# Kernel optimization log

Hardware: AMD Instinct MI355X
Metric: run time of the kernel (lower is better)

Reference implementation:

```python
import jax, jax.numpy as jnp
import numpy as np
import math

B, T, D, H, E, K = 2, 2048, 1024, 16, 8, 2
F = 4 * D
HD = D // H
EPS = 1e-5


def layer_norm(x, w):
    mu = jnp.mean(x, axis=-1, keepdims=True)
    var = jnp.mean(jnp.square(x - mu), axis=-1, keepdims=True)
    return (x - mu) / jnp.sqrt(var + EPS) * w


def setup_inputs() -> dict:
    key = jax.random.key(0)
    ks = jax.random.split(key, 8)
    s = 0.02
    return {
        "x": jax.random.normal(ks[0], (B, T, D), dtype=jnp.float32),
        "ln1_w": jnp.ones((D,), dtype=jnp.float32),
        "wqkv": jax.random.normal(ks[1], (D, 3 * D), dtype=jnp.float32) * s,
        "wproj": jax.random.normal(ks[2], (D, D), dtype=jnp.float32) * s,
        "ln2_w": jnp.ones((D,), dtype=jnp.float32),
        "router_w": jax.random.normal(ks[3], (D, E), dtype=jnp.float32) * s,
        "w1": jax.random.normal(ks[4], (E, D, F), dtype=jnp.float32) * s,
        "w2": jax.random.normal(ks[5], (E, F, D), dtype=jnp.float32) * s,
    }


def reference(x, ln1_w, wqkv, wproj, ln2_w, router_w, w1, w2):
    # --- self-attention (causal, no bias, dropout=0, eval mode) ---
    h = layer_norm(x, ln1_w)
    qkv = h @ wqkv  # [B,T,3D]
    q, k, v = jnp.split(qkv, 3, axis=-1)
    q = q.reshape(B, T, H, HD).transpose(0, 2, 1, 3)  # [B,H,T,HD]
    k = k.reshape(B, T, H, HD).transpose(0, 2, 1, 3)
    v = v.reshape(B, T, H, HD).transpose(0, 2, 1, 3)
    scores = jnp.einsum("bhqd,bhkd->bhqk", q, k) / math.sqrt(HD)
    causal = jnp.tril(jnp.ones((T, T), dtype=bool))
    scores = jnp.where(causal, scores, jnp.float32(-1e9))
    attn = jax.nn.softmax(scores, axis=-1)
    o = jnp.einsum("bhqk,bhkd->bhqd", attn, v)
    o = o.transpose(0, 2, 1, 3).reshape(B, T, D) @ wproj
    x = x + o

    # --- pre-MoE norm (note: residual for MoE uses ln2 output, per source) ---
    x = layer_norm(x, ln2_w)

    # --- router (eval mode: top-k of softmax probs) ---
    logits = x @ router_w  # [B,T,E]
    probs = jax.nn.softmax(logits, axis=-1)
    _, topi = jax.lax.top_k(probs, K)  # [B,T,K]
    mask = jax.nn.one_hot(topi, E, dtype=probs.dtype).sum(axis=-2)  # [B,T,E]
    rp = probs * mask
    rp = rp / jnp.sum(rp, axis=-1, keepdims=True)  # normalize=True, top_k>1

    # --- experts: dense-equivalent of gather/MLP/scatter (zero-prob tokens contribute 0) ---
    hh = jax.nn.gelu(jnp.einsum("btd,edf->ebtf", x, w1), approximate=False)
    eo = jnp.einsum("ebtf,efd->ebtd", hh, w2)
    next_states = jnp.einsum("bte,ebtd->btd", rp, eo)
    return x + next_states
```

## Files before the change

kernel.cpp:

```cpp
#include <hip/hip_runtime.h>
#include <hip/hip_bf16.h>
#include <math.h>

#define Bv 2
#define Tv 2048
#define Dv 1024
#define Hv 16
#define Ev 8
#define Kv 2
#define Fv 4096
#define HDv 64
#define NT 4096
#define MAXTILES 72

typedef __attribute__((ext_vector_type(8))) short short8;
typedef __attribute__((ext_vector_type(4))) float f32x4;

__device__ __forceinline__ short f2bf(float f) {
  unsigned u = __builtin_bit_cast(unsigned, f);
  u += 0x7fffu + ((u >> 16) & 1u);
  return (short)(u >> 16);
}
__device__ __forceinline__ float bf2f(short s) {
  unsigned u = ((unsigned)(unsigned short)s) << 16;
  return __builtin_bit_cast(float, u);
}
__device__ __forceinline__ float wredsum(float s) {
  #pragma unroll
  for (int off = 32; off; off >>= 1) s += __shfl_down(s, off, 64);
  return s;
}
__device__ __forceinline__ void gl_lds16(const short* g, short* l) {
  __builtin_amdgcn_global_load_lds(
      (const __attribute__((address_space(1))) unsigned int*)g,
      (__attribute__((address_space(3))) unsigned int*)l, 16, 0, 0);
}

__global__ __launch_bounds__(256) void transpose_cvt(const float* __restrict__ in,
                                                     short* __restrict__ out,
                                                     int Kd, int Nd) {
  __shared__ float tile[64][65];
  const float* inb = in + (size_t)blockIdx.z * Kd * Nd;
  short* outb = out + (size_t)blockIdx.z * Kd * Nd;
  const int k0 = blockIdx.x * 64, n0 = blockIdx.y * 64;
  const int rr = threadIdx.x >> 4, cc = (threadIdx.x & 15) * 4;
  #pragma unroll
  for (int i = 0; i < 4; i++) {
    int r = rr + i * 16;
    f32x4 v = *(const f32x4*)(inb + (size_t)(k0 + r) * Nd + n0 + cc);
    tile[r][cc] = v[0]; tile[r][cc + 1] = v[1];
    tile[r][cc + 2] = v[2]; tile[r][cc + 3] = v[3];
  }
  __syncthreads();
  #pragma unroll
  for (int i = 0; i < 2; i++) {
    int e = threadIdx.x + i * 256;
    int n = e >> 3, c = (e & 7) * 8;
    short8 v;
    #pragma unroll
    for (int j = 0; j < 8; j++) v[j] = f2bf(tile[c + j][n]);
    *(short8*)(outb + (size_t)(n0 + n) * Kd + k0 + c) = v;
  }
}

__global__ __launch_bounds__(256) void vtrans_kernel(const short* __restrict__ qkv,
                                                     short* __restrict__ vT) {
  __shared__ short tile[64][72];
  const int t0 = blockIdx.x * 64;
  const int bh = blockIdx.y;
  const int b = bh >> 4, h = bh & 15;
  #pragma unroll
  for (int i = 0; i < 2; i++) {
    int e = threadIdx.x + i * 256;
    int r = e >> 3, c = (e & 7) * 8;
    short8 v = *(const short8*)(qkv + (size_t)(b * Tv + t0 + r) * 3072 + 2048 + h * 64 + c);
    *(short8*)(&tile[r][c]) = v;
  }
  __syncthreads();
  #pragma unroll
  for (int i = 0; i < 2; i++) {
    int e = threadIdx.x + i * 256;
    int d = e >> 3, c = (e & 7) * 8;
    short8 v;
    #pragma unroll
    for (int j = 0; j < 8; j++) v[j] = tile[c + j][d];
    *(short8*)(vT + ((size_t)bh * 64 + d) * Tv + t0 + c) = v;
  }
}

__global__ __launch_bounds__(256) void ln_kernel(const float* __restrict__ in,
                                                 const float* __restrict__ w,
                                                 float* __restrict__ outf,
                                                 short* __restrict__ outb) {
  int t = blockIdx.x;
  int tid = threadIdx.x;
  const float* row = in + (size_t)t * Dv;
  float v[4]; float s = 0.f;
  #pragma unroll
  for (int i = 0; i < 4; i++) { v[i] = row[tid + i * 256]; s += v[i]; }
  s = wredsum(s);
  __shared__ float red[4], red2[4];
  int wv = tid >> 6, ln = tid & 63;
  if (ln == 0) red[wv] = s;
  __syncthreads();
  float mu = (red[0] + red[1] + red[2] + red[3]) * (1.f / Dv);
  float vs = 0.f;
  #pragma unroll
  for (int i = 0; i < 4; i++) { float d = v[i] - mu; vs += d * d; }
  vs = wredsum(vs);
  if (ln == 0) red2[wv] = vs;
  __syncthreads();
  float var = (red2[0] + red2[1] + red2[2] + red2[3]) * (1.f / Dv);
  float inv = rsqrtf(var + 1e-5f);
  #pragma unroll
  for (int i = 0; i < 4; i++) {
    int d = tid + i * 256;
    float o = (v[i] - mu) * inv * w[d];
    if (outf) outf[(size_t)t * Dv + d] = o;
    if (outb) outb[(size_t)t * Dv + d] = f2bf(o);
  }
}

enum { EPI_BF16 = 0, EPI_RESID = 1, EPI_GELU = 2, EPI_F32 = 3 };

template<int EPI, bool MOE, bool INDIRECT>
__global__ __launch_bounds__(256) void gemm_lds(
    const short* __restrict__ A, const short* __restrict__ Bt,
    short* __restrict__ Cb, float* __restrict__ Cf,
    const float* __restrict__ resid,
    const int* __restrict__ perm, const int* __restrict__ tiles,
    int M, int N, int K) {
  __shared__ short As[128][32];
  __shared__ short Bs[128][32];
  const int nwg = gridDim.x * gridDim.y;
  const int orig = blockIdx.y * gridDim.x + blockIdx.x;
  const int cpx = nwg >> 3;
  const int wgid = (orig & 7) * cpx + (orig >> 3);
  const int mt = wgid % gridDim.x;
  const int npan = wgid / gridDim.x;

  int row0, row_end;
  const short* Bp = Bt;
  if (MOE) {
    int ntile = tiles[0];
    if (mt >= ntile) return;
    int e   = tiles[1 + mt * 3];
    row0    = tiles[2 + mt * 3];
    row_end = tiles[3 + mt * 3];
    Bp = Bt + (size_t)e * K * N;
  } else {
    row0 = mt * 128; row_end = M;
  }
  const int nbase = npan * 128;
  const int tid = threadIdx.x;
  const int lane = tid & 63;
  const int w = tid >> 6;
  const int wm = (w >> 1) * 64, wn = (w & 1) * 64;
  const int lr = lane & 15, lk = (lane >> 4) * 8;

  const int lrow = lane >> 2, lcol = (lane & 3) * 8;
  const short* asrc[2]; short* adst[2];
  const short* bsrc[2]; short* bdst[2];
  #pragma unroll
  for (int i = 0; i < 2; i++) {
    int grow = row0 + w * 16 + i * 64 + lrow;
    if (MOE) grow = min(grow, row_end - 1);
    int arow = INDIRECT ? perm[grow] : grow;
    asrc[i] = A + (size_t)arow * K + lcol;
    adst[i] = &As[w * 16 + i * 64][0];
    bsrc[i] = Bp + (size_t)(nbase + w * 16 + i * 64 + lrow) * K + lcol;
    bdst[i] = &Bs[w * 16 + i * 64][0];
  }

  f32x4 acc[4][4];
  #pragma unroll
  for (int m = 0; m < 4; m++)
    #pragma unroll
    for (int n = 0; n < 4; n++) acc[m][n] = (f32x4)0.0f;

  for (int k0 = 0; k0 < K; k0 += 32) {
    #pragma unroll
    for (int i = 0; i < 2; i++) {
      gl_lds16(asrc[i] + k0, adst[i]);
      gl_lds16(bsrc[i] + k0, bdst[i]);
    }
    __syncthreads();
    short8 af[4], bfr[4];
    #pragma unroll
    for (int m = 0; m < 4; m++) af[m] = *(const short8*)(&As[wm + m * 16 + lr][lk]);
    #pragma unroll
    for (int n = 0; n < 4; n++) bfr[n] = *(const short8*)(&Bs[wn + n * 16 + lr][lk]);
    #pragma unroll
    for (int m = 0; m < 4; m++)
      #pragma unroll
      for (int n = 0; n < 4; n++)
        acc[m][n] = __builtin_amdgcn_mfma_f32_16x16x32_bf16(af[m], bfr[n], acc[m][n], 0, 0, 0);
    __syncthreads();
  }
  #pragma unroll
  for (int m = 0; m < 4; m++) {
    #pragma unroll
    for (int n = 0; n < 4; n++) {
      #pragma unroll
      for (int r = 0; r < 4; r++) {
        int row = row0 + wm + m * 16 + (lane >> 4) * 4 + r;
        if (MOE && row >= row_end) continue;
        int col = nbase + wn + n * 16 + lr;
        float v = acc[m][n][r];
        size_t idx = (size_t)row * N + col;
        if (EPI == EPI_BF16) {
          Cb[idx] = f2bf(v);
        } else if (EPI == EPI_RESID) {
          Cf[idx] = v + resid[idx];
        } else if (EPI == EPI_GELU) {
          float g = 0.5f * v * (1.0f + erff(v * 0.70710678118f));
          Cb[idx] = f2bf(g);
        } else {
          Cf[idx] = v;
        }
      }
    }
  }
}

#define SCL2E 0.18033688011112042f

__global__ __launch_bounds__(256) void attn_kernel(const short* __restrict__ qkv,
                                                   const short* __restrict__ vT,
                                                   short* __restrict__ o) {
  const int qbase = ((int)gridDim.x - 1 - (int)blockIdx.x) * 64;
  const int bh = blockIdx.y;
  const int b = bh >> 4, h = bh & 15;
  const int w = threadIdx.x >> 6, lane = threadIdx.x & 63;
  const int lr = lane & 15, lkg = lane >> 4, lk = lkg * 8;
  const size_t rs = 3 * Dv;

  __shared__ short Ks[64][72];
  __shared__ short Vs[64][72];
  __shared__ short Ps[4][16][72];

  short8 qf[2];
  {
    size_t qrow = (size_t)(b * Tv + qbase + w * 16 + lr) * rs + h * 64;
    qf[0] = *(const short8*)(qkv + qrow + lk);
    qf[1] = *(const short8*)(qkv + qrow + 32 + lk);
  }
  f32x4 oacc[4];
  #pragma unroll
  for (int n = 0; n < 4; n++) oacc[n] = (f32x4)0.0f;
  float mrow[4] = {-INFINITY, -INFINITY, -INFINITY, -INFINITY};
  float lrow4[4] = {0.f, 0.f, 0.f, 0.f};

  const short* kbase = qkv + (size_t)b * Tv * rs + Dv + h * 64;
  const short* vbase = vT + (size_t)bh * 64 * Tv;

  for (int kv0 = 0; kv0 < qbase + 64; kv0 += 64) {
    #pragma unroll
    for (int i = 0; i < 2; i++) {
      int e = threadIdx.x + i * 256;
      int r = e >> 3, c = (e & 7) * 8;
      short8 kval = *(const short8*)(kbase + (size_t)(kv0 + r) * rs + c);
      *(short8*)(&Ks[r][c]) = kval;
      short8 vval = *(const short8*)(vbase + (size_t)r * Tv + kv0 + c);
      *(short8*)(&Vs[r][c]) = vval;
    }
    __syncthreads();
    f32x4 s[4];
    #pragma unroll
    for (int n = 0; n < 4; n++) {
      s[n] = (f32x4)0.0f;
      short8 kf0 = *(const short8*)(&Ks[n * 16 + lr][lk]);
      short8 kf1 = *(const short8*)(&Ks[n * 16 + lr][32 + lk]);
      s[n] = __builtin_amdgcn_mfma_f32_16x16x32_bf16(qf[0], kf0, s[n], 0, 0, 0);
      s[n] = __builtin_amdgcn_mfma_f32_16x16x32_bf16(qf[1], kf1, s[n], 0, 0, 0);
    }
    if (kv0 < qbase) {
      #pragma unroll
      for (int n = 0; n < 4; n++)
        #pragma unroll
        for (int r = 0; r < 4; r++) s[n][r] *= SCL2E;
    } else {
      #pragma unroll
      for (int n = 0; n < 4; n++)
        #pragma unroll
        for (int r = 0; r < 4; r++) {
          int tq = qbase + w * 16 + lkg * 4 + r;
          int tk = kv0 + n * 16 + lr;
          s[n][r] = (tk > tq) ? -1e30f : s[n][r] * SCL2E;
        }
    }
    float scr[4];
    #pragma unroll
    for (int r = 0; r < 4; r++) {
      float m = fmaxf(fmaxf(s[0][r], s[1][r]), fmaxf(s[2][r], s[3][r]));
      #pragma unroll
      for (int off = 8; off; off >>= 1) m = fmaxf(m, __shfl_xor(m, off, 64));
      float mnew = fmaxf(mrow[r], m);
      float sc = exp2f(mrow[r] - mnew);
      float rsum = 0.f;
      #pragma unroll
      for (int n = 0; n < 4; n++) { float p = exp2f(s[n][r] - mnew); s[n][r] = p; rsum += p; }
      #pragma unroll
      for (int off = 8; off; off >>= 1) rsum += __shfl_xor(rsum, off, 64);
      lrow4[r] = lrow4[r] * sc + rsum;
      mrow[r] = mnew;
      scr[r] = sc;
    }
    #pragma unroll
    for (int n = 0; n < 4; n++)
      #pragma unroll
      for (int r = 0; r < 4; r++) Ps[w][lkg * 4 + r][n * 16 + lr] = f2bf(s[n][r]);
    #pragma unroll
    for (int n = 0; n < 4; n++)
      #pragma unroll
      for (int r = 0; r < 4; r++) oacc[n][r] *= scr[r];
    __syncthreads();
    #pragma unroll
    for (int n2 = 0; n2 < 4; n2++) {
      short8 pf0 = *(const short8*)(&Ps[w][lr][lk]);
      short8 pf1 = *(const short8*)(&Ps[w][lr][32 + lk]);
      short8 vf0 = *(const short8*)(&Vs[n2 * 16 + lr][lk]);
      short8 vf1 = *(const short8*)(&Vs[n2 * 16 + lr][32 + lk]);
      oacc[n2] = __builtin_amdgcn_mfma_f32_16x16x32_bf16(pf0, vf0, oacc[n2], 0, 0, 0);
      oacc[n2] = __builtin_amdgcn_mfma_f32_16x16x32_bf16(pf1, vf1, oacc[n2], 0, 0, 0);
    }
    __syncthreads();
  }
  float rinv[4];
  #pragma unroll
  for (int r = 0; r < 4; r++) rinv[r] = 1.0f / lrow4[r];
  #pragma unroll
  for (int n2 = 0; n2 < 4; n2++)
    #pragma unroll
    for (int r = 0; r < 4; r++) {
      int tq = qbase + w * 16 + lkg * 4 + r;
      float v = oacc[n2][r] * rinv[r];
      o[(size_t)(b * Tv + tq) * Dv + h * 64 + n2 * 16 + lr] = f2bf(v);
    }
}

__global__ __launch_bounds__(256) void router_kernel(const float* __restrict__ x2f,
                                                     const float* __restrict__ rw,
                                                     int* __restrict__ topi,
                                                     float* __restrict__ topp) {
  int w = threadIdx.x >> 6, lane = threadIdx.x & 63;
  int t = blockIdx.x * 4 + w;
  const float* row = x2f + (size_t)t * Dv;
  float acc[8];
  #pragma unroll
  for (int e = 0; e < 8; e++) acc[e] = 0.f;
  for (int i = 0; i < 16; i++) {
    int d = lane + i * 64;
    float xv = row[d];
    const float* rwp = rw + (size_t)d * 8;
    #pragma unroll
    for (int e = 0; e < 8; e++) acc[e] += xv * rwp[e];
  }
  #pragma unroll
  for (int e = 0; e < 8; e++) acc[e] = wredsum(acc[e]);
  if (lane == 0) {
    float mx = acc[0];
    #pragma unroll
    for (int e = 1; e < 8; e++) mx = fmaxf(mx, acc[e]);
    float p[8]; float se = 0.f;
    #pragma unroll
    for (int e = 0; e < 8; e++) { p[e] = expf(acc[e] - mx); se += p[e]; }
    #pragma unroll
    for (int e = 0; e < 8; e++) p[e] /= se;
    int i1 = 0; float p1 = p[0];
    #pragma unroll
    for (int e = 1; e < 8; e++) if (p[e] > p1) { p1 = p[e]; i1 = e; }
    float pm = p[i1]; p[i1] = -1.f;
    int i2 = 0; float p2 = p[0];
    #pragma unroll
    for (int e = 1; e < 8; e++) if (p[e] > p2) { p2 = p[e]; i2 = e; }
    float sum = pm + p2;
    topi[t * 2] = i1; topi[t * 2 + 1] = i2;
    topp[t * 2] = pm / sum; topp[t * 2 + 1] = p2 / sum;
  }
}

__global__ void bucket_count(const int* __restrict__ topi, int* __restrict__ offsets,
                             int* __restrict__ cursor) {
  __shared__ int cnt[8];
  if (threadIdx.x < 8) { cnt[threadIdx.x] = 0; cursor[threadIdx.x] = 0; }
  __syncthreads();
  for (int i = threadIdx.x; i < NT * 2; i += 256) atomicAdd(&cnt[topi[i]], 1);
  __syncthreads();
  if (threadIdx.x == 0) {
    int s = 0;
    for (int e = 0; e < 8; e++) { offsets[e] = s; s += cnt[e]; }
    offsets[8] = s;
  }
}
__global__ void bucket_scatter(const int* __restrict__ topi, const int* __restrict__ offsets,
                               int* __restrict__ cursor, int* __restrict__ perm,
                               int* __restrict__ row_of) {
  int i = blockIdx.x * 256 + threadIdx.x;
  if (i >= NT * 2) return;
  int e = topi[i];
  int slot = atomicAdd(&cursor[e], 1);
  int r = offsets[e] + slot;
  perm[r] = i >> 1;
  row_of[i] = r;
}
__global__ void tile_build(const int* __restrict__ offsets, int* __restrict__ tiles) {
  if (threadIdx.x == 0 && blockIdx.x == 0) {
    int nt = 0;
    for (int e = 0; e < 8; e++) {
      int r0 = offsets[e], r1 = offsets[e + 1];
      for (int m = r0; m < r1; m += 128) {
        tiles[1 + nt * 3] = e; tiles[2 + nt * 3] = m; tiles[3 + nt * 3] = r1; nt++;
      }
    }
    tiles[0] = nt;
  }
}

__global__ __launch_bounds__(256) void final_kernel(float* __restrict__ out,
                                                    const short* __restrict__ eout,
                                                    const int* __restrict__ row_of,
                                                    const float* __restrict__ topp) {
  int t = blockIdx.x; int tid = threadIdx.x;
  int r0 = row_of[t * 2], r1 = row_of[t * 2 + 1];
  float p0 = topp[t * 2], p1 = topp[t * 2 + 1];
  #pragma unroll
  for (int i = 0; i < 4; i++) {
    int d = tid + i * 256;
    out[(size_t)t * Dv + d] += p0 * bf2f(eout[(size_t)r0 * Dv + d])
                             + p1 * bf2f(eout[(size_t)r1 * Dv + d]);
  }
}

extern "C" void kernel_launch(void* const* d_in, const int* in_sizes, int n_in,
                              void* d_out, int out_size, void* d_ws, size_t ws_size,
                              hipStream_t stream) {
  const float* x        = (const float*)d_in[0];
  const float* ln1_w    = (const float*)d_in[1];
  const float* wqkv     = (const float*)d_in[2];
  const float* wproj    = (const float*)d_in[3];
  const float* ln2_w    = (const float*)d_in[4];
  const float* router_w = (const float*)d_in[5];
  const float* w1       = (const float*)d_in[6];
  const float* w2       = (const float*)d_in[7];
  float* out = (float*)d_out;
  char* ws = (char*)d_ws;

  size_t off = 0;
  short* wqkvT  = (short*)(ws + off); off += (size_t)3 * Dv * Dv * 2;
  short* wprojT = (short*)(ws + off); off += (size_t)Dv * Dv * 2;
  short* w1T    = (short*)(ws + off); off += (size_t)Ev * Dv * Fv * 2;
  short* w2T    = (short*)(ws + off); off += (size_t)Ev * Fv * Dv * 2;
  char* reg1 = ws + off; off += (size_t)NT * Dv * 2;
  short* hln1 = (short*)reg1;
  short* ob   = (short*)reg1;
  short* x2b  = (short*)reg1;
  char* reg2 = ws + off; off += (size_t)NT * 3 * Dv * 2;
  short* qkvb = (short*)reg2;
  float* xres = (float*)reg2;
  char* reg3 = ws + off; off += (size_t)NT * 2 * Fv * 2;
  short* vT = (short*)reg3;
  short* Hb = (short*)reg3;
  short* eout = (short*)(ws + off); off += (size_t)NT * 2 * Dv * 2;
  int*   topi = (int*)(ws + off);   off += NT * 2 * 4;
  float* topp = (float*)(ws + off); off += NT * 2 * 4;
  int*   offs = (int*)(ws + off);   off += 64;
  int*   cur  = (int*)(ws + off);   off += 64;
  int*   perm = (int*)(ws + off);   off += NT * 2 * 4;
  int*   rowof= (int*)(ws + off);   off += NT * 2 * 4;
  int*   tiles= (int*)(ws + off);   off += 1024;

  transpose_cvt<<<dim3(Dv / 64, 3 * Dv / 64, 1), 256, 0, stream>>>(wqkv, wqkvT, Dv, 3 * Dv);
  transpose_cvt<<<dim3(Dv / 64, Dv / 64, 1), 256, 0, stream>>>(wproj, wprojT, Dv, Dv);
  transpose_cvt<<<dim3(Dv / 64, Fv / 64, Ev), 256, 0, stream>>>(w1, w1T, Dv, Fv);
  transpose_cvt<<<dim3(Fv / 64, Dv / 64, Ev), 256, 0, stream>>>(w2, w2T, Fv, Dv);

  ln_kernel<<<NT, 256, 0, stream>>>(x, ln1_w, nullptr, hln1);
  gemm_lds<EPI_BF16, false, false><<<dim3(NT / 128, 3 * Dv / 128), 256, 0, stream>>>(
      hln1, wqkvT, qkvb, nullptr, nullptr, nullptr, nullptr, NT, 3 * Dv, Dv);
  vtrans_kernel<<<dim3(Tv / 64, Bv * Hv), 256, 0, stream>>>(qkvb, vT);
  attn_kernel<<<dim3(Tv / 64, Bv * Hv), 256, 0, stream>>>(qkvb, vT, ob);
  gemm_lds<EPI_RESID, false, false><<<dim3(NT / 128, Dv / 128), 256, 0, stream>>>(
      ob, wprojT, nullptr, xres, x, nullptr, nullptr, NT, Dv, Dv);
  ln_kernel<<<NT, 256, 0, stream>>>(xres, ln2_w, out, x2b);
  router_kernel<<<NT / 4, 256, 0, stream>>>(out, router_w, topi, topp);
  bucket_count<<<1, 256, 0, stream>>>(topi, offs, cur);
  bucket_scatter<<<NT * 2 / 256, 256, 0, stream>>>(topi, offs, cur, perm, rowof);
  tile_build<<<1, 1, 0, stream>>>(offs, tiles);
  gemm_lds<EPI_GELU, true, true><<<dim3(MAXTILES, Fv / 128), 256, 0, stream>>>(
      x2b, w1T, Hb, nullptr, nullptr, perm, tiles, 0, Fv, Dv);
  gemm_lds<EPI_BF16, true, false><<<dim3(MAXTILES, Dv / 128), 256, 0, stream>>>(
      Hb, w2T, eout, nullptr, nullptr, nullptr, tiles, 0, Dv, Fv);
  final_kernel<<<NT, 256, 0, stream>>>(out, eout, rowof, topp);
}
```

Measured before the change: 654.7 us.

## Split-K the projection and MoE down-projection GEMMs with bf16 partials

Adds a SPLITK template parameter to the GEMM so the attention output projection and the MoE second GEMM run with two K-slices along grid z. Each slice writes bf16 partials, which a new resid_combine kernel (projection) and the final combine kernel (experts) sum. The goal is more workgroups on the low-occupancy N=1024 GEMMs, in particular the long-K (4096) expert down-projection. The cost is an extra kernel, extra partial-buffer traffic, and bf16 rounding of the projection partials before the residual add, where the old code used an fp32 epilogue.

```diff
diff --git a/kernel.cpp b/kernel.cpp
--- a/kernel.cpp
+++ b/kernel.cpp
@@ -121,13 +121,12 @@
   }
 }
 
-enum { EPI_BF16 = 0, EPI_RESID = 1, EPI_GELU = 2, EPI_F32 = 3 };
-
-template<int EPI, bool MOE, bool INDIRECT>
+enum { EPI_BF16 = 0, EPI_GELU = 2 };
+
+template<int EPI, bool MOE, bool INDIRECT, int SPLITK>
 __global__ __launch_bounds__(256) void gemm_lds(
     const short* __restrict__ A, const short* __restrict__ Bt,
-    short* __restrict__ Cb, float* __restrict__ Cf,
-    const float* __restrict__ resid,
+    short* __restrict__ Cb,
     const int* __restrict__ perm, const int* __restrict__ tiles,
     int M, int N, int K) {
   __shared__ short As[128][32];
@@ -151,6 +150,10 @@
   } else {
     row0 = mt * 128; row_end = M;
   }
+  const int kslice = K / SPLITK;
+  const int kz = (SPLITK > 1) ? (int)blockIdx.z * kslice : 0;
+  short* Cout = Cb + ((SPLITK > 1) ? (size_t)blockIdx.z * M * N : 0);
+
   const int nbase = npan * 128;
   const int tid = threadIdx.x;
   const int lane = tid & 63;
@@ -166,9 +169,9 @@
     int grow = row0 + w * 16 + i * 64 + lrow;
     if (MOE) grow = min(grow, row_end - 1);
     int arow = INDIRECT ? perm[grow] : grow;
-    asrc[i] = A + (size_t)arow * K + lcol;
+    asrc[i] = A + (size_t)arow * K + kz + lcol;
     adst[i] = &As[w * 16 + i * 64][0];
-    bsrc[i] = Bp + (size_t)(nbase + w * 16 + i * 64 + lrow) * K + lcol;
+    bsrc[i] = Bp + (size_t)(nbase + w * 16 + i * 64 + lrow) * K + kz + lcol;
     bdst[i] = &Bs[w * 16 + i * 64][0];
   }
 
@@ -178,7 +181,7 @@
     #pragma unroll
     for (int n = 0; n < 4; n++) acc[m][n] = (f32x4)0.0f;
 
-  for (int k0 = 0; k0 < K; k0 += 32) {
+  for (int k0 = 0; k0 < kslice; k0 += 32) {
     #pragma unroll
     for (int i = 0; i < 2; i++) {
       gl_lds16(asrc[i] + k0, adst[i]);
@@ -208,18 +211,26 @@
         int col = nbase + wn + n * 16 + lr;
         float v = acc[m][n][r];
         size_t idx = (size_t)row * N + col;
-        if (EPI == EPI_BF16) {
-          Cb[idx] = f2bf(v);
-        } else if (EPI == EPI_RESID) {
-          Cf[idx] = v + resid[idx];
-        } else if (EPI == EPI_GELU) {
+        if (EPI == EPI_GELU) {
           float g = 0.5f * v * (1.0f + erff(v * 0.70710678118f));
-          Cb[idx] = f2bf(g);
+          Cout[idx] = f2bf(g);
         } else {
-          Cf[idx] = v;
+          Cout[idx] = f2bf(v);
         }
       }
     }
+  }
+}
+
+__global__ __launch_bounds__(256) void resid_combine(float* __restrict__ xres,
+                                                     const float* __restrict__ x,
+                                                     const short* __restrict__ p) {
+  size_t i = (size_t)blockIdx.x * 1024 + threadIdx.x;
+  const size_t mn = (size_t)NT * Dv;
+  #pragma unroll
+  for (int j = 0; j < 4; j++) {
+    size_t idx = i + (size_t)j * 256;
+    xres[idx] = x[idx] + bf2f(p[idx]) + bf2f(p[idx + mn]);
   }
 }
 
@@ -424,11 +435,13 @@
   int t = blockIdx.x; int tid = threadIdx.x;
   int r0 = row_of[t * 2], r1 = row_of[t * 2 + 1];
   float p0 = topp[t * 2], p1 = topp[t * 2 + 1];
+  const size_t mn = (size_t)NT * 2 * Dv;
   #pragma unroll
   for (int i = 0; i < 4; i++) {
     int d = tid + i * 256;
-    out[(size_t)t * Dv + d] += p0 * bf2f(eout[(size_t)r0 * Dv + d])
-                             + p1 * bf2f(eout[(size_t)r1 * Dv + d]);
+    size_t i0 = (size_t)r0 * Dv + d, i1 = (size_t)r1 * Dv + d;
+    out[(size_t)t * Dv + d] += p0 * (bf2f(eout[i0]) + bf2f(eout[i0 + mn]))
+                             + p1 * (bf2f(eout[i1]) + bf2f(eout[i1 + mn]));
   }
 }
 
@@ -459,9 +472,10 @@
   short* qkvb = (short*)reg2;
   float* xres = (float*)reg2;
   char* reg3 = ws + off; off += (size_t)NT * 2 * Fv * 2;
-  short* vT = (short*)reg3;
-  short* Hb = (short*)reg3;
-  short* eout = (short*)(ws + off); off += (size_t)NT * 2 * Dv * 2;
+  short* vT    = (short*)reg3;
+  short* pproj = (short*)reg3;
+  short* Hb    = (short*)reg3;
+  short* eout = (short*)(ws + off); off += (size_t)2 * NT * 2 * Dv * 2;
   int*   topi = (int*)(ws + off);   off += NT * 2 * 4;
   float* topp = (float*)(ws + off); off += NT * 2 * 4;
   int*   offs = (int*)(ws + off);   off += 64;
@@ -476,20 +490,21 @@
   transpose_cvt<<<dim3(Fv / 64, Dv / 64, Ev), 256, 0, stream>>>(w2, w2T, Fv, Dv);
 
   ln_kernel<<<NT, 256, 0, stream>>>(x, ln1_w, nullptr, hln1);
-  gemm_lds<EPI_BF16, false, false><<<dim3(NT / 128, 3 * Dv / 128), 256, 0, stream>>>(
-      hln1, wqkvT, qkvb, nullptr, nullptr, nullptr, nullptr, NT, 3 * Dv, Dv);
+  gemm_lds<EPI_BF16, false, false, 1><<<dim3(NT / 128, 3 * Dv / 128), 256, 0, stream>>>(
+      hln1, wqkvT, qkvb, nullptr, nullptr, NT, 3 * Dv, Dv);
   vtrans_kernel<<<dim3(Tv / 64, Bv * Hv), 256, 0, stream>>>(qkvb, vT);
   attn_kernel<<<dim3(Tv / 64, Bv * Hv), 256, 0, stream>>>(qkvb, vT, ob);
-  gemm_lds<EPI_RESID, false, false><<<dim3(NT / 128, Dv / 128), 256, 0, stream>>>(
-      ob, wprojT, nullptr, xres, x, nullptr, nullptr, NT, Dv, Dv);
+  gemm_lds<EPI_BF16, false, false, 2><<<dim3(NT / 128, Dv / 128, 2), 256, 0, stream>>>(
+      ob, wprojT, pproj, nullptr, nullptr, NT, Dv, Dv);
+  resid_combine<<<NT, 256, 0, stream>>>(xres, x, pproj);
   ln_kernel<<<NT, 256, 0, stream>>>(xres, ln2_w, out, x2b);
   router_kernel<<<NT / 4, 256, 0, stream>>>(out, router_w, topi, topp);
   bucket_count<<<1, 256, 0, stream>>>(topi, offs, cur);
   bucket_scatter<<<NT * 2 / 256, 256, 0, stream>>>(topi, offs, cur, perm, rowof);
   tile_build<<<1, 1, 0, stream>>>(offs, tiles);
-  gemm_lds<EPI_GELU, true, true><<<dim3(MAXTILES, Fv / 128), 256, 0, stream>>>(
-      x2b, w1T, Hb, nullptr, nullptr, perm, tiles, 0, Fv, Dv);
-  gemm_lds<EPI_BF16, true, false><<<dim3(MAXTILES, Dv / 128), 256, 0, stream>>>(
-      Hb, w2T, eout, nullptr, nullptr, nullptr, tiles, 0, Dv, Fv);
+  gemm_lds<EPI_GELU, true, true, 1><<<dim3(MAXTILES, Fv / 128), 256, 0, stream>>>(
+      x2b, w1T, Hb, perm, tiles, NT * 2, Fv, Dv);
+  gemm_lds<EPI_BF16, true, false, 2><<<dim3(MAXTILES, Dv / 128, 2), 256, 0, stream>>>(
+      Hb, w2T, eout, nullptr, tiles, NT * 2, Dv, Fv);
   final_kernel<<<NT, 256, 0, stream>>>(out, eout, rowof, topp);
 }
```

Result: no change. 656.8 us (+0.3%).

## Use 256-row double-buffered GEMM kernel for MoE expert matmuls

Applied to the files above, without the earlier changes.

Adds a new 512-thread GEMM kernel for the two expert GEMMs. It uses 256-row M tiles, N tiles of 256 or 128, K steps of 64, and double-buffered LDS so the next tile's global-to-LDS load overlaps the MFMA work on the current one. Tile building now steps by 256 rows and the grid uses 40 M-tiles. The aim is more data reuse per tile, fewer syncs and better latency hiding, at the cost of larger LDS use per block, more padding waste in partially filled expert tiles, and possibly lower occupancy.

```diff
diff --git a/kernel.cpp b/kernel.cpp
--- a/kernel.cpp
+++ b/kernel.cpp
@@ -11,7 +11,7 @@
 #define Fv 4096
 #define HDv 64
 #define NT 4096
-#define MAXTILES 72
+#define MT256 40
 
 typedef __attribute__((ext_vector_type(8))) short short8;
 typedef __attribute__((ext_vector_type(4))) float f32x4;
@@ -121,14 +121,13 @@
   }
 }
 
-enum { EPI_BF16 = 0, EPI_RESID = 1, EPI_GELU = 2, EPI_F32 = 3 };
-
-template<int EPI, bool MOE, bool INDIRECT>
+enum { EPI_BF16 = 0, EPI_RESID = 1, EPI_GELU = 2 };
+
+template<int EPI>
 __global__ __launch_bounds__(256) void gemm_lds(
     const short* __restrict__ A, const short* __restrict__ Bt,
     short* __restrict__ Cb, float* __restrict__ Cf,
     const float* __restrict__ resid,
-    const int* __restrict__ perm, const int* __restrict__ tiles,
     int M, int N, int K) {
   __shared__ short As[128][32];
   __shared__ short Bs[128][32];
@@ -139,18 +138,7 @@
   const int mt = wgid % gridDim.x;
   const int npan = wgid / gridDim.x;
 
-  int row0, row_end;
-  const short* Bp = Bt;
-  if (MOE) {
-    int ntile = tiles[0];
-    if (mt >= ntile) return;
-    int e   = tiles[1 + mt * 3];
-    row0    = tiles[2 + mt * 3];
-    row_end = tiles[3 + mt * 3];
-    Bp = Bt + (size_t)e * K * N;
-  } else {
-    row0 = mt * 128; row_end = M;
-  }
+  const int row0 = mt * 128;
   const int nbase = npan * 128;
   const int tid = threadIdx.x;
   const int lane = tid & 63;
@@ -163,12 +151,9 @@
   const short* bsrc[2]; short* bdst[2];
   #pragma unroll
   for (int i = 0; i < 2; i++) {
-    int grow = row0 + w * 16 + i * 64 + lrow;
-    if (MOE) grow = min(grow, row_end - 1);
-    int arow = INDIRECT ? perm[grow] : grow;
-    asrc[i] = A + (size_t)arow * K + lcol;
+    asrc[i] = A + (size_t)(row0 + w * 16 + i * 64 + lrow) * K + lcol;
     adst[i] = &As[w * 16 + i * 64][0];
-    bsrc[i] = Bp + (size_t)(nbase + w * 16 + i * 64 + lrow) * K + lcol;
+    bsrc[i] = Bt + (size_t)(nbase + w * 16 + i * 64 + lrow) * K + lcol;
     bdst[i] = &Bs[w * 16 + i * 64][0];
   }
 
@@ -204,19 +189,122 @@
       #pragma unroll
       for (int r = 0; r < 4; r++) {
         int row = row0 + wm + m * 16 + (lane >> 4) * 4 + r;
-        if (MOE && row >= row_end) continue;
         int col = nbase + wn + n * 16 + lr;
         float v = acc[m][n][r];
         size_t idx = (size_t)row * N + col;
-        if (EPI == EPI_BF16) {
+        if (EPI == EPI_RESID) {
+          Cf[idx] = v + resid[idx];
+        } else {
           Cb[idx] = f2bf(v);
-        } else if (EPI == EPI_RESID) {
-          Cf[idx] = v + resid[idx];
-        } else if (EPI == EPI_GELU) {
+        }
+      }
+    }
+  }
+}
+
+template<int BN, int EPI, bool INDIRECT>
+__global__ __launch_bounds__(512, 2) void gemm2ph256(
+    const short* __restrict__ A, const short* __restrict__ Bt,
+    short* __restrict__ Cb,
+    const int* __restrict__ perm, const int* __restrict__ tiles,
+    int N, int K) {
+  constexpr int WN = (BN == 256) ? 4 : 2;
+  constexpr int WM = 8 / WN;
+  constexpr int MR = 256 / WM / 16;
+  constexpr int BI = BN / 64;
+  __shared__ short As[2][256][64];
+  __shared__ short Bs[2][BN][64];
+
+  const int nwg = gridDim.x * gridDim.y;
+  const int orig = blockIdx.y * gridDim.x + blockIdx.x;
+  const int cpx = nwg >> 3;
+  const int wgid = (orig & 7) * cpx + (orig >> 3);
+  const int mt = wgid % gridDim.x;
+  const int npan = wgid / gridDim.x;
+
+  const int ntile = tiles[0];
+  if (mt >= ntile) return;
+  const int e   = tiles[1 + mt * 3];
+  const int row0    = tiles[2 + mt * 3];
+  const int row_end = tiles[3 + mt * 3];
+  const short* Bp = Bt + (size_t)e * K * N;
+
+  const int nbase = npan * BN;
+  const int tid = threadIdx.x;
+  const int lane = tid & 63;
+  const int wv = tid >> 6;
+  const int wm = (wv / WN) * (MR * 16);
+  const int wn = (wv % WN) * 64;
+  const int lr = lane & 15, lk = (lane >> 4) * 8;
+
+  const int srow = lane >> 3;
+  const int scol = (lane & 7) * 8;
+  const short* aptr[4];
+  #pragma unroll
+  for (int i = 0; i < 4; i++) {
+    int grow = row0 + wv * 32 + i * 8 + srow;
+    grow = min(grow, row_end - 1);
+    int arow = INDIRECT ? perm[grow] : grow;
+    aptr[i] = A + (size_t)arow * K + scol;
+  }
+  const short* bptr[BI];
+  #pragma unroll
+  for (int i = 0; i < BI; i++)
+    bptr[i] = Bp + (size_t)(nbase + wv * (BN / 8) + i * 8 + srow) * K + scol;
+
+  f32x4 acc[MR][4];
+  #pragma unroll
+  for (int m = 0; m < MR; m++)
+    #pragma unroll
+    for (int n = 0; n < 4; n++) acc[m][n] = (f32x4)0.0f;
+
+  const int KT = K >> 6;
+  #pragma unroll
+  for (int i = 0; i < 4; i++) gl_lds16(aptr[i], &As[0][wv * 32 + i * 8][0]);
+  #pragma unroll
+  for (int i = 0; i < BI; i++) gl_lds16(bptr[i], &Bs[0][wv * (BN / 8) + i * 8][0]);
+  __syncthreads();
+  int cur = 0;
+  for (int kt = 0; kt < KT; ++kt) {
+    if (kt + 1 < KT) {
+      const int k0 = (kt + 1) << 6;
+      #pragma unroll
+      for (int i = 0; i < 4; i++) gl_lds16(aptr[i] + k0, &As[cur ^ 1][wv * 32 + i * 8][0]);
+      #pragma unroll
+      for (int i = 0; i < BI; i++) gl_lds16(bptr[i] + k0, &Bs[cur ^ 1][wv * (BN / 8) + i * 8][0]);
+    }
+    #pragma unroll
+    for (int kk = 0; kk < 64; kk += 32) {
+      short8 af[MR], bfr[4];
+      #pragma unroll
+      for (int m = 0; m < MR; m++) af[m] = *(const short8*)(&As[cur][wm + m * 16 + lr][kk + lk]);
+      #pragma unroll
+      for (int n = 0; n < 4; n++) bfr[n] = *(const short8*)(&Bs[cur][wn + n * 16 + lr][kk + lk]);
+      #pragma unroll
+      for (int m = 0; m < MR; m++)
+        #pragma unroll
+        for (int n = 0; n < 4; n++)
+          acc[m][n] = __builtin_amdgcn_mfma_f32_16x16x32_bf16(af[m], bfr[n], acc[m][n], 0, 0, 0);
+    }
+    __syncthreads();
+    cur ^= 1;
+  }
+  #pragma unroll
+  for (int m = 0; m < MR; m++) {
+    #pragma unroll
+    for (int n = 0; n < 4; n++) {
+      #pragma unroll
+      for (int r = 0; r < 4; r++) {
+        int row = row0 + wm + m * 16 + (lane >> 4) * 4 + r;
+        if (row >= row_end) continue;
+        int col = nbase + wn + n * 16 + lr;
+        float v = acc[m][n][r];
+        size_t idx = (size_t)row * N + col;
+        if (EPI == EPI_GELU) {
           float g = 0.5f * v * (1.0f + erff(v * 0.70710678118f));
           Cb[idx] = f2bf(g);
         } else {
-          Cf[idx] = v;
+          Cb[idx] = f2bf(v);
         }
       }
     }
@@ -409,7 +497,7 @@
     int nt = 0;
     for (int e = 0; e < 8; e++) {
       int r0 = offsets[e], r1 = offsets[e + 1];
-      for (int m = r0; m < r1; m += 128) {
+      for (int m = r0; m < r1; m += 256) {
         tiles[1 + nt * 3] = e; tiles[2 + nt * 3] = m; tiles[3 + nt * 3] = r1; nt++;
       }
     }
@@ -476,20 +564,20 @@
   transpose_cvt<<<dim3(Fv / 64, Dv / 64, Ev), 256, 0, stream>>>(w2, w2T, Fv, Dv);
 
   ln_kernel<<<NT, 256, 0, stream>>>(x, ln1_w, nullptr, hln1);
-  gemm_lds<EPI_BF16, false, false><<<dim3(NT / 128, 3 * Dv / 128), 256, 0, stream>>>(
-      hln1, wqkvT, qkvb, nullptr, nullptr, nullptr, nullptr, NT, 3 * Dv, Dv);
+  gemm_lds<EPI_BF16><<<dim3(NT / 128, 3 * Dv / 128), 256, 0, stream>>>(
+      hln1, wqkvT, qkvb, nullptr, nullptr, NT, 3 * Dv, Dv);
   vtrans_kernel<<<dim3(Tv / 64, Bv * Hv), 256, 0, stream>>>(qkvb, vT);
   attn_kernel<<<dim3(Tv / 64, Bv * Hv), 256, 0, stream>>>(qkvb, vT, ob);
-  gemm_lds<EPI_RESID, false, false><<<dim3(NT / 128, Dv / 128), 256, 0, stream>>>(
-      ob, wprojT, nullptr, xres, x, nullptr, nullptr, NT, Dv, Dv);
+  gemm_lds<EPI_RESID><<<dim3(NT / 128, Dv / 128), 256, 0, stream>>>(
+      ob, wprojT, nullptr, xres, x, NT, Dv, Dv);
   ln_kernel<<<NT, 256, 0, stream>>>(xres, ln2_w, out, x2b);
   router_kernel<<<NT / 4, 256, 0, stream>>>(out, router_w, topi, topp);
   bucket_count<<<1, 256, 0, stream>>>(topi, offs, cur);
   bucket_scatter<<<NT * 2 / 256, 256, 0, stream>>>(topi, offs, cur, perm, rowof);
   tile_build<<<1, 1, 0, stream>>>(offs, tiles);
-  gemm_lds<EPI_GELU, true, true><<<dim3(MAXTILES, Fv / 128), 256, 0, stream>>>(
-      x2b, w1T, Hb, nullptr, nullptr, perm, tiles, 0, Fv, Dv);
-  gemm_lds<EPI_BF16, true, false><<<dim3(MAXTILES, Dv / 128), 256, 0, stream>>>(
-      Hb, w2T, eout, nullptr, nullptr, nullptr, tiles, 0, Dv, Fv);
+  gemm2ph256<256, EPI_GELU, true><<<dim3(MT256, Fv / 256), 512, 0, stream>>>(
+      x2b, w1T, Hb, perm, tiles, Fv, Dv);
+  gemm2ph256<128, EPI_BF16, false><<<dim3(MT256, Dv / 128), 512, 0, stream>>>(
+      Hb, w2T, eout, perm, tiles, Dv, Fv);
   final_kernel<<<NT, 256, 0, stream>>>(out, eout, rowof, topp);
 }
```

Result: slower. 759.1 us (+15.9%).
